# Kernel optimization log

Hardware: AMD Instinct MI355X
Metric: run time of the kernel (lower is better)

The kernel has to match this reference:

```python
import jax, jax.numpy as jnp
import numpy as np

B, N, K = 4, 512, 10
PI_SCALE = 0.05  # keeps sum_k pi in (0, 0.5) so the [1e-8, 1] clamp does not saturate at 1
MCMC_KEY = jax.random.key(42)


def setup_inputs() -> dict:
    key = jax.random.key(0)
    k1, k2, k3, k4 = jax.random.split(key, 4)
    mu = jax.random.normal(k1, (B, N, K), dtype=jnp.float32)
    sig = jax.random.uniform(k2, (B, N, K), dtype=jnp.float32)
    pi = jax.random.uniform(k3, (B, N, K), dtype=jnp.float32) * PI_SCALE
    A_0 = jax.random.uniform(k4, (N, N), dtype=jnp.float32)
    return {"mu": mu, "sig": sig, "pi": pi, "A_0": A_0, "num_samples": 100}


def reference(mu, sig, pi, A_0, num_samples):
    b, n, k = mu.shape

    # Mixture-weighted proposal mean/std:  sum_k softmax(pi)_k * {mu,sig}_k
    component_probs = jax.nn.softmax(pi, axis=-1)          # [B,N,K]
    selected_mu = jnp.sum(component_probs * mu, axis=-1)    # [B,N]
    selected_sig = jnp.sum(component_probs * sig, axis=-1)  # [B,N]

    # edge_probs[b,i,j] = clamp(sum_k pi[b,i,k]) -- constant in j; hoisted out of the loop
    # since it depends only on pi (the torch code recomputes it every step).
    edge_probs = jnp.clip(jnp.sum(pi, axis=2), 1e-8, 1.0)[:, :, None]  # [B,N,1]
    log_ep = jnp.log(edge_probs)                                        # [B,N,1]
    log_1mep = jnp.log(1.0 - edge_probs)                                # [B,N,1]

    def log_likelihood(A):  # A: [B,N,N] -> [N]  (sum over dims 0,1 as in torch)
        return jnp.sum(A * log_ep + (1.0 - A) * log_1mep, axis=(0, 1))

    def step(carry, t):
        current_A, acc = carry
        kk = jax.random.fold_in(MCMC_KEY, t)
        k_noise, k_unif = jax.random.split(kk)
        noise = jax.random.normal(k_noise, (b, n), dtype=selected_mu.dtype)
        proposed_mu = selected_mu + noise * selected_sig              # [B,N]
        # sigmoid of rank-1 outer product: einsum('bnc,bmc->bnm') with c==1
        proposed_A = jax.nn.sigmoid(proposed_mu[:, :, None] * proposed_mu[:, None, :])
        ratio = jnp.mean(jnp.clip(jnp.exp(log_likelihood(proposed_A) - log_likelihood(current_A)), 0.0, 1.0))
        accept = jax.random.uniform(k_unif, (b,)) < ratio             # [B] bool
        current_A = jnp.where(accept[:, None, None], proposed_A, current_A)
        return (current_A, acc + current_A), None

    cur0 = jnp.broadcast_to(A_0, (b, n, n)).astype(mu.dtype)
    acc0 = jnp.zeros((b, n, n), dtype=mu.dtype)
    (_, acc), _ = jax.lax.scan(step, (cur0, acc0), jnp.arange(num_samples))
    return acc / num_samples
```

## Files before the change

### kernel.cpp

```cpp
#include <hip/hip_runtime.h>
#include <stdint.h>

#define T_STEPS 100
#define BB 4
#define NN 512
#define KK 10
#define LOG2E 1.4426950408889634

typedef float f4 __attribute__((ext_vector_type(4)));

__device__ __forceinline__ uint32_t rotl32(uint32_t v, int d) {
  return (v << d) | (v >> (32 - d));
}

__device__ __forceinline__ void tf2x32(uint32_t k0, uint32_t k1,
                                       uint32_t& x0, uint32_t& x1) {
  uint32_t k2 = k0 ^ k1 ^ 0x1BD11BDAu;
  x0 += k0; x1 += k1;
#define TFR(r) { x0 += x1; x1 = rotl32(x1, r); x1 ^= x0; }
  TFR(13) TFR(15) TFR(26) TFR(6)   x0 += k1; x1 += k2 + 1u;
  TFR(17) TFR(29) TFR(16) TFR(24)  x0 += k2; x1 += k0 + 2u;
  TFR(13) TFR(15) TFR(26) TFR(6)   x0 += k0; x1 += k1 + 3u;
  TFR(17) TFR(29) TFR(16) TFR(24)  x0 += k1; x1 += k2 + 4u;
  TFR(13) TFR(15) TFR(26) TFR(6)   x0 += k2; x1 += k0 + 5u;
#undef TFR
}

__device__ __forceinline__ float bits_to_u01(uint32_t bits) {
  return __fsub_rn(__uint_as_float((bits >> 9) | 0x3f800000u), 1.0f);
}

__device__ __forceinline__ float erfinv_f32(float x) {
  float w = -logf(__fmul_rn(__fsub_rn(1.0f, x), __fadd_rn(1.0f, x)));
  float p;
  if (w < 5.0f) {
    w = __fsub_rn(w, 2.5f);
    p = 2.81022636e-08f;
    p = __fadd_rn(__fmul_rn(p, w), 3.43273939e-07f);
    p = __fadd_rn(__fmul_rn(p, w), -3.5233877e-06f);
    p = __fadd_rn(__fmul_rn(p, w), -4.39150654e-06f);
    p = __fadd_rn(__fmul_rn(p, w), 0.00021858087f);
    p = __fadd_rn(__fmul_rn(p, w), -0.00125372503f);
    p = __fadd_rn(__fmul_rn(p, w), -0.00417768164f);
    p = __fadd_rn(__fmul_rn(p, w), 0.246640727f);
    p = __fadd_rn(__fmul_rn(p, w), 1.50140941f);
  } else {
    w = __fsub_rn(sqrtf(w), 3.0f);
    p = -0.000200214257f;
    p = __fadd_rn(__fmul_rn(p, w), 0.000100950558f);
    p = __fadd_rn(__fmul_rn(p, w), 0.00134934322f);
    p = __fadd_rn(__fmul_rn(p, w), -0.00367342844f);
    p = __fadd_rn(__fmul_rn(p, w), 0.00573950773f);
    p = __fadd_rn(__fmul_rn(p, w), -0.0076224613f);
    p = __fadd_rn(__fmul_rn(p, w), 0.00943887047f);
    p = __fadd_rn(__fmul_rn(p, w), 1.00167406f);
    p = __fadd_rn(__fmul_rn(p, w), 2.83297682f);
  }
  return __fmul_rn(p, x);
}

__device__ __forceinline__ float fast_sigmoid(float x) {
  float e = __expf(-x);
  return __builtin_amdgcn_rcpf(__fadd_rn(1.0f, e));
}

template <int CTRL>
__device__ __forceinline__ float dpp_add(float x) {
  int v = __builtin_amdgcn_update_dpp(0, __float_as_int(x), CTRL, 0xF, 0xF, true);
  return __fadd_rn(x, __int_as_float(v));
}
__device__ __forceinline__ float readlane_f(float x, int lane) {
  return __int_as_float(__builtin_amdgcn_readlane(__float_as_int(x), lane));
}

__global__ void rng_kernel(const float* __restrict__ mu,
                           const float* __restrict__ sig,
                           const float* __restrict__ pi,
                           float* __restrict__ pm, float* __restrict__ uacc,
                           float* __restrict__ Lf) {
  int id = blockIdx.x * blockDim.x + threadIdx.x;
  if (id >= T_STEPS * BB * NN) return;
  int t = id >> 11;
  int m = id & 2047;

  const float* pp = pi + m * KK;
  float mx = pp[0];
  for (int k = 1; k < KK; k++) mx = fmaxf(mx, pp[k]);
  float e[KK]; float s = 0.0f;
  for (int k = 0; k < KK; k++) { e[k] = expf(__fsub_rn(pp[k], mx)); s = __fadd_rn(s, e[k]); }
  float smv = 0.0f, ssv = 0.0f, eps = 0.0f;
  for (int k = 0; k < KK; k++) {
    float p = e[k] / s;
    smv = __fadd_rn(smv, __fmul_rn(p, mu[m * KK + k]));
    ssv = __fadd_rn(ssv, __fmul_rn(p, sig[m * KK + k]));
    eps = __fadd_rn(eps, pp[k]);
  }
  if (t == 0) {
    float ep = fminf(fmaxf(eps, 1e-8f), 1.0f);
    float lep = logf(ep);
    float l1 = logf(__fsub_rn(1.0f, ep));
    Lf[m] = (float)((double)lep - (double)l1);
  }

  uint32_t kk0 = 0u, kk1 = (uint32_t)t;
  tf2x32(0u, 42u, kk0, kk1);
  uint32_t n0 = 0u, n1 = 0u; tf2x32(kk0, kk1, n0, n1);
  uint32_t y0 = 0u, y1 = (uint32_t)m;
  tf2x32(n0, n1, y0, y1);
  uint32_t bits = y0 ^ y1;

  float u01 = bits_to_u01(bits);
  const float lo = -0.99999994f;
  float u = fmaxf(lo, __fadd_rn(__fmul_rn(u01, 2.0f), lo));
  float z = __fmul_rn(1.41421356237309515f, erfinv_f32(u));
  pm[id] = __fadd_rn(smv, __fmul_rn(z, ssv));

  if (m < 4) {
    uint32_t u0 = 0u, u1 = 1u; tf2x32(kk0, kk1, u0, u1);
    uint32_t c0 = 0u, c1 = (uint32_t)m;
    tf2x32(u0, u1, c0, c1);
    uacc[t * 4 + m] = __fmul_rn(bits_to_u01(c0 ^ c1), 512.0f);
  }
}

__global__ __launch_bounds__(512) void ll_kernel(const float* __restrict__ pm,
                                                 const float* __restrict__ Lf,
                                                 const float* __restrict__ A0,
                                                 float* __restrict__ llt,
                                                 float* __restrict__ ll0,
                                                 float* __restrict__ tsum) {
  __shared__ float spm[BB][NN];
  __shared__ float sL[BB][NN];
  __shared__ double pt[4][128];
  int tid = threadIdx.x;
  int q = tid >> 7, jj = tid & 127;
  int bi = blockIdx.x;
  if (bi < 400) {
    int t = bi >> 2, jc = bi & 3;
    #pragma unroll
    for (int b = 0; b < BB; b++) {
      spm[b][tid] = pm[(t * 4 + b) * NN + tid];
      sL[b][tid] = Lf[b * NN + tid];
    }
    __syncthreads();
    int i0 = q * 128;
    double tsd = 0.0;
    for (int b = 0; b < BB; b++) {
      float pmj = spm[b][jc * 128 + jj];
      double acc = 0.0;
      #pragma unroll 8
      for (int i = 0; i < 128; i += 2) {
        float x0 = __fmul_rn(spm[b][i0 + i], pmj);
        float x1 = __fmul_rn(spm[b][i0 + i + 1], pmj);
        float t0 = __fmul_rn(fast_sigmoid(x0), sL[b][i0 + i]);
        float t1 = __fmul_rn(fast_sigmoid(x1), sL[b][i0 + i + 1]);
        acc += (double)__fadd_rn(t0, t1);
      }
      pt[q][jj] = acc;
      __syncthreads();
      if (tid < 128) {
        double a = ((pt[0][jj] + pt[1][jj]) + pt[2][jj]) + pt[3][jj];
        llt[(t * 4 + b) * NN + jc * 128 + jj] = (float)(a * LOG2E);
        tsd += a;
      }
      __syncthreads();
    }
    if (tid < 128) tsum[t * NN + jc * 128 + jj] = (float)(tsd * LOG2E);
  } else {
    int idx = bi - 400;
    int b = idx >> 2, jc = idx & 3;
    sL[0][tid] = Lf[b * NN + tid];
    __syncthreads();
    int j = jc * 128 + jj;
    int i0 = q * 128;
    double acc = 0.0;
    #pragma unroll 4
    for (int i = 0; i < 128; i++) {
      acc += (double)A0[(size_t)(i0 + i) * NN + j] * (double)sL[0][i0 + i];
    }
    pt[q][jj] = acc;
    __syncthreads();
    if (tid < 128) {
      double a = ((pt[0][jj] + pt[1][jj]) + pt[2][jj]) + pt[3][jj];
      ll0[b * NN + jc * 128 + jj] = (float)(a * LOG2E);
    }
  }
}

#define CH_LOAD(BUF, T)                                                      \
  {                                                                          \
    BUF##Ts0 = tsv[(size_t)(T) * 128 + g];                                   \
    BUF##Ts1 = tsv[(size_t)(T) * 128 + 64 + g];                              \
    _Pragma("unroll")                                                        \
    for (int b = 0; b < 4; b++) {                                            \
      _Pragma("unroll")                                                      \
      for (int k = 0; k < 2; k++)                                            \
        BUF##R[b * 2 + k] = lltv[((size_t)(T) * 4 + b) * 128 + k * 64 + g];  \
    }                                                                        \
  }

#define CH_STEP(BUF, T)                                                      \
  {                                                                          \
    float4 ua = sua[T];                                                      \
    f4 d0 = BUF##Ts0 - C0;                                                   \
    f4 d1 = BUF##Ts1 - C1;                                                   \
    f4 E0, E1;                                                               \
    _Pragma("unroll")                                                        \
    for (int c = 0; c < 4; c++) {                                            \
      E0[c] = fminf(exp2f(d0[c]), 1.0f);                                     \
      E1[c] = fminf(exp2f(d1[c]), 1.0f);                                     \
    }                                                                        \
    f4 Es = E0 + E1;                                                         \
    float ps = __fadd_rn(__fadd_rn(Es[0], Es[1]), __fadd_rn(Es[2], Es[3]));  \
    ps = dpp_add<0xB1>(ps);                                        \
    ps = dpp_add<0x4E>(ps);                                        \
    ps = dpp_add<0x141>(ps);                         \
    ps = dpp_add<0x140>(ps);                              \
    float s0 = readlane_f(ps, 0), s1 = readlane_f(ps, 16);                   \
    float s2 = readlane_f(ps, 32), s3 = readlane_f(ps, 48);                  \
    float tot = __fadd_rn(__fadd_rn(s0, s1), __fadd_rn(s2, s3));             \
    int am = (ua.x < tot ? 1 : 0) | (ua.y < tot ? 2 : 0) |                   \
             (ua.z < tot ? 4 : 0) | (ua.w < tot ? 8 : 0);                    \
    am = __builtin_amdgcn_readfirstlane(am);                                 \
    if (am) {                                                                \
      if (am & 1) { st0 = (T); cur[0] = BUF##R[0]; cur[1] = BUF##R[1]; }     \
      if (am & 2) { st1 = (T); cur[2] = BUF##R[2]; cur[3] = BUF##R[3]; }     \
      if (am & 4) { st2 = (T); cur[4] = BUF##R[4]; cur[5] = BUF##R[5]; }     \
      if (am & 8) { st3 = (T); cur[6] = BUF##R[6]; cur[7] = BUF##R[7]; }     \
      C0 = (cur[0] + cur[2]) + (cur[4] + cur[6]);                            \
      C1 = (cur[1] + cur[3]) + (cur[5] + cur[7]);                            \
    }                                                                        \
    if (g == 0) {                                                            \
      uint32_t pk = (uint32_t)(st0 + 1) | ((uint32_t)(st1 + 1) << 8) |       \
                    ((uint32_t)(st2 + 1) << 16) | ((uint32_t)(st3 + 1) << 24);\
      spk[T] = pk;                                                           \
    }                                                                        \
  }

__global__ __launch_bounds__(64, 1) void chain_kernel(const float* __restrict__ llt,
                                                      const float* __restrict__ tsum,
                                                      const float* __restrict__ ll0,
                                                      const float* __restrict__ uacc,
                                                      int* __restrict__ slist,
                                                      float* __restrict__ wlist,
                                                      int* __restrict__ Mv) {
  __shared__ float4 sua[T_STEPS];
  __shared__ uint32_t spk[T_STEPS];
  __shared__ int scnt[BB][101];
  int g = threadIdx.x;

  const float4* uacc4 = (const float4*)uacc;
  for (int t = g; t < T_STEPS; t += 64) sua[t] = uacc4[t];

  const f4* lltv = (const f4*)llt;
  const f4* tsv  = (const f4*)tsum;
  const f4* ll0v = (const f4*)ll0;

  f4 cur[8];
  #pragma unroll
  for (int b = 0; b < 4; b++)
    #pragma unroll
    for (int k = 0; k < 2; k++) cur[b * 2 + k] = ll0v[b * 128 + k * 64 + g];
  f4 C0 = (cur[0] + cur[2]) + (cur[4] + cur[6]);
  f4 C1 = (cur[1] + cur[3]) + (cur[5] + cur[7]);
  int st0 = -1, st1 = -1, st2 = -1, st3 = -1;

  f4 ATs0, ATs1, AR[8];
  f4 BTs0, BTs1, BR[8];
  CH_LOAD(A, 0)
  CH_LOAD(B, 1)
  __syncthreads();

  for (int t = 0; t < T_STEPS; t += 2) {
    CH_STEP(A, t)
    if (t + 2 < T_STEPS) CH_LOAD(A, t + 2)
    CH_STEP(B, t + 1)
    if (t + 3 < T_STEPS) CH_LOAD(B, t + 3)
  }

  __syncthreads();
  for (int s = g; s < BB * 101; s += 64) (&scnt[0][0])[s] = 0;
  __syncthreads();
  {
    uint32_t p0 = spk[g];
    atomicAdd(&scnt[0][p0 & 255], 1);
    atomicAdd(&scnt[1][(p0 >> 8) & 255], 1);
    atomicAdd(&scnt[2][(p0 >> 16) & 255], 1);
    atomicAdd(&scnt[3][p0 >> 24], 1);
    if (g < T_STEPS - 64) {
      uint32_t p1 = spk[64 + g];
      atomicAdd(&scnt[0][p1 & 255], 1);
      atomicAdd(&scnt[1][(p1 >> 8) & 255], 1);
      atomicAdd(&scnt[2][(p1 >> 16) & 255], 1);
      atomicAdd(&scnt[3][p1 >> 24], 1);
    }
  }
  __syncthreads();
  if (g < 4) {
    int m = 0;
    for (int s = 0; s <= 100; s++) {
      int c = scnt[g][s];
      if (c) { slist[g * 104 + m] = s; wlist[g * 104 + m] = (float)c; m++; }
    }
    Mv[g] = m;
  }
}

__global__ __launch_bounds__(512) void out_kernel(const float* __restrict__ pm,
                                                  const float* __restrict__ A0,
                                                  const int* __restrict__ slist,
                                                  const float* __restrict__ wlist,
                                                  const int* __restrict__ Mv,
                                                  float* __restrict__ out) {
  int b = blockIdx.x >> 9;
  int i = blockIdx.x & 511;
  int j = threadIdx.x;
  int M = Mv[b];
  float r = 0.0f;
  for (int e = 0; e < M; e++) {
    int s = slist[b * 104 + e];
    float w = wlist[b * 104 + e];
    if (s == 0) {
      r += w * A0[(size_t)i * NN + j];
    } else {
      int t = s - 1;
      float pmi = pm[(size_t)(t * BB + b) * NN + i];
      float pmj = pm[(size_t)(t * BB + b) * NN + j];
      r += w * fast_sigmoid(__fmul_rn(pmi, pmj));
    }
  }
  out[((size_t)b * NN + i) * NN + j] = r * 0.01f;
}

extern "C" void kernel_launch(void* const* d_in, const int* in_sizes, int n_in,
                              void* d_out, int out_size, void* d_ws, size_t ws_size,
                              hipStream_t stream) {
  const float* mu  = (const float*)d_in[0];
  const float* sig = (const float*)d_in[1];
  const float* pi  = (const float*)d_in[2];
  const float* A0  = (const float*)d_in[3];

  char* ws = (char*)d_ws;
  size_t off = 0;
  auto alloc = [&](size_t bytes) -> char* {
    char* p = ws + off;
    off += (bytes + 255) & ~(size_t)255;
    return p;
  };
  float* llt   = (float*)alloc((size_t)T_STEPS * BB * NN * 4);
  float* tsum  = (float*)alloc((size_t)T_STEPS * NN * 4);
  float* ll0   = (float*)alloc(BB * NN * 4);
  float* pm    = (float*)alloc((size_t)T_STEPS * BB * NN * 4);
  float* Lf    = (float*)alloc(BB * NN * 4);
  float* uacc  = (float*)alloc(T_STEPS * 4 * 4);
  int*   slist = (int*)alloc(BB * 104 * 4);
  float* wlist = (float*)alloc(BB * 104 * 4);
  int*   Mv    = (int*)alloc(4 * 4);
  float* outp  = (float*)d_out;

  rng_kernel<<<(T_STEPS * BB * NN + 255) / 256, 256, 0, stream>>>(mu, sig, pi,
                                                                  pm, uacc, Lf);
  ll_kernel<<<416, 512, 0, stream>>>(pm, Lf, A0, llt, ll0, tsum);
  chain_kernel<<<1, 64, 0, stream>>>(llt, tsum, ll0, uacc, slist, wlist, Mv);
  out_kernel<<<BB * NN, 512, 0, stream>>>(pm, A0, slist, wlist, Mv, outp);
}
```

Measured before the change: 155.4 us.

## Fuse RNG into likelihood kernel and process two chain steps speculatively per iteration

Removes the separate rng_kernel by computing the softmax-weighted proposal means, noise, log-odds and uniforms inside ll_kernel's prologue. Each of the four column blocks recomputes this for its timestep, and only jc==0 writes pm. The serial chain kernel now handles steps in pairs. It speculatively evaluates the second step's acceptance ratio for every possible number of batch acceptances in the first step, ordered by uniform rank, so the two wave reductions no longer depend on each other. This cuts a kernel launch and shortens the serial dependency chain, at the cost of redundant RNG/softmax work and about six reductions per pair instead of two.

```diff
diff --git a/kernel.cpp b/kernel.cpp
--- a/kernel.cpp
+++ b/kernel.cpp
@@ -72,60 +72,32 @@
 __device__ __forceinline__ float readlane_f(float x, int lane) {
   return __int_as_float(__builtin_amdgcn_readlane(__float_as_int(x), lane));
 }
-
-__global__ void rng_kernel(const float* __restrict__ mu,
-                           const float* __restrict__ sig,
-                           const float* __restrict__ pi,
-                           float* __restrict__ pm, float* __restrict__ uacc,
-                           float* __restrict__ Lf) {
-  int id = blockIdx.x * blockDim.x + threadIdx.x;
-  if (id >= T_STEPS * BB * NN) return;
-  int t = id >> 11;
-  int m = id & 2047;
-
-  const float* pp = pi + m * KK;
-  float mx = pp[0];
-  for (int k = 1; k < KK; k++) mx = fmaxf(mx, pp[k]);
-  float e[KK]; float s = 0.0f;
-  for (int k = 0; k < KK; k++) { e[k] = expf(__fsub_rn(pp[k], mx)); s = __fadd_rn(s, e[k]); }
-  float smv = 0.0f, ssv = 0.0f, eps = 0.0f;
-  for (int k = 0; k < KK; k++) {
-    float p = e[k] / s;
-    smv = __fadd_rn(smv, __fmul_rn(p, mu[m * KK + k]));
-    ssv = __fadd_rn(ssv, __fmul_rn(p, sig[m * KK + k]));
-    eps = __fadd_rn(eps, pp[k]);
-  }
-  if (t == 0) {
-    float ep = fminf(fmaxf(eps, 1e-8f), 1.0f);
-    float lep = logf(ep);
-    float l1 = logf(__fsub_rn(1.0f, ep));
-    Lf[m] = (float)((double)lep - (double)l1);
-  }
-
-  uint32_t kk0 = 0u, kk1 = (uint32_t)t;
-  tf2x32(0u, 42u, kk0, kk1);
-  uint32_t n0 = 0u, n1 = 0u; tf2x32(kk0, kk1, n0, n1);
-  uint32_t y0 = 0u, y1 = (uint32_t)m;
-  tf2x32(n0, n1, y0, y1);
-  uint32_t bits = y0 ^ y1;
-
-  float u01 = bits_to_u01(bits);
-  const float lo = -0.99999994f;
-  float u = fmaxf(lo, __fadd_rn(__fmul_rn(u01, 2.0f), lo));
-  float z = __fmul_rn(1.41421356237309515f, erfinv_f32(u));
-  pm[id] = __fadd_rn(smv, __fmul_rn(z, ssv));
-
-  if (m < 4) {
-    uint32_t u0 = 0u, u1 = 1u; tf2x32(kk0, kk1, u0, u1);
-    uint32_t c0 = 0u, c1 = (uint32_t)m;
-    tf2x32(u0, u1, c0, c1);
-    uacc[t * 4 + m] = __fmul_rn(bits_to_u01(c0 ^ c1), 512.0f);
-  }
-}
-
-__global__ __launch_bounds__(512) void ll_kernel(const float* __restrict__ pm,
-                                                 const float* __restrict__ Lf,
+__device__ __forceinline__ float wave_tot(float ps) {
+  ps = dpp_add<0xB1>(ps);
+  ps = dpp_add<0x4E>(ps);
+  ps = dpp_add<0x141>(ps);
+  ps = dpp_add<0x140>(ps);
+  float s0 = readlane_f(ps, 0), s1 = readlane_f(ps, 16);
+  float s2 = readlane_f(ps, 32), s3 = readlane_f(ps, 48);
+  return __fadd_rn(__fadd_rn(s0, s1), __fadd_rn(s2, s3));
+}
+__device__ __forceinline__ float eval8(f4 a0, f4 a1) {
+  f4 E0, E1;
+  #pragma unroll
+  for (int c = 0; c < 4; c++) {
+    E0[c] = fminf(exp2f(a0[c]), 1.0f);
+    E1[c] = fminf(exp2f(a1[c]), 1.0f);
+  }
+  f4 Es = E0 + E1;
+  return __fadd_rn(__fadd_rn(Es[0], Es[1]), __fadd_rn(Es[2], Es[3]));
+}
+
+__global__ __launch_bounds__(512) void ll_kernel(const float* __restrict__ mu,
+                                                 const float* __restrict__ sig,
+                                                 const float* __restrict__ pi,
                                                  const float* __restrict__ A0,
+                                                 float* __restrict__ pm,
+                                                 float* __restrict__ uacc,
                                                  float* __restrict__ llt,
                                                  float* __restrict__ ll0,
                                                  float* __restrict__ tsum) {
@@ -137,10 +109,45 @@
   int bi = blockIdx.x;
   if (bi < 400) {
     int t = bi >> 2, jc = bi & 3;
+    uint32_t kk0 = 0u, kk1 = (uint32_t)t;
+    tf2x32(0u, 42u, kk0, kk1);
+    uint32_t n0 = 0u, n1 = 0u; tf2x32(kk0, kk1, n0, n1);
     #pragma unroll
     for (int b = 0; b < BB; b++) {
-      spm[b][tid] = pm[(t * 4 + b) * NN + tid];
-      sL[b][tid] = Lf[b * NN + tid];
+      int m = b * NN + tid;
+      const float* pp = pi + m * KK;
+      float mx = pp[0];
+      for (int k = 1; k < KK; k++) mx = fmaxf(mx, pp[k]);
+      float e[KK]; float s = 0.0f;
+      for (int k = 0; k < KK; k++) { e[k] = expf(__fsub_rn(pp[k], mx)); s = __fadd_rn(s, e[k]); }
+      float smv = 0.0f, ssv = 0.0f, eps = 0.0f;
+      for (int k = 0; k < KK; k++) {
+        float p = e[k] / s;
+        smv = __fadd_rn(smv, __fmul_rn(p, mu[m * KK + k]));
+        ssv = __fadd_rn(ssv, __fmul_rn(p, sig[m * KK + k]));
+        eps = __fadd_rn(eps, pp[k]);
+      }
+      float ep = fminf(fmaxf(eps, 1e-8f), 1.0f);
+      float lep = logf(ep);
+      float l1 = logf(__fsub_rn(1.0f, ep));
+      sL[b][tid] = (float)((double)lep - (double)l1);
+
+      uint32_t y0 = 0u, y1 = (uint32_t)m;
+      tf2x32(n0, n1, y0, y1);
+      uint32_t bits = y0 ^ y1;
+      float u01 = bits_to_u01(bits);
+      const float lo = -0.99999994f;
+      float u = fmaxf(lo, __fadd_rn(__fmul_rn(u01, 2.0f), lo));
+      float z = __fmul_rn(1.41421356237309515f, erfinv_f32(u));
+      float pmv = __fadd_rn(smv, __fmul_rn(z, ssv));
+      spm[b][tid] = pmv;
+      if (jc == 0) pm[(t * 4 + b) * NN + tid] = pmv;
+    }
+    if (jc == 0 && tid < 4) {
+      uint32_t u0 = 0u, u1 = 1u; tf2x32(kk0, kk1, u0, u1);
+      uint32_t c0 = 0u, c1 = (uint32_t)tid;
+      tf2x32(u0, u1, c0, c1);
+      uacc[t * 4 + tid] = __fmul_rn(bits_to_u01(c0 ^ c1), 512.0f);
     }
     __syncthreads();
     int i0 = q * 128;
@@ -169,7 +176,16 @@
   } else {
     int idx = bi - 400;
     int b = idx >> 2, jc = idx & 3;
-    sL[0][tid] = Lf[b * NN + tid];
+    {
+      int m = b * NN + tid;
+      const float* pp = pi + m * KK;
+      float eps = 0.0f;
+      for (int k = 0; k < KK; k++) eps = __fadd_rn(eps, pp[k]);
+      float ep = fminf(fmaxf(eps, 1e-8f), 1.0f);
+      float lep = logf(ep);
+      float l1 = logf(__fsub_rn(1.0f, ep));
+      sL[0][tid] = (float)((double)lep - (double)l1);
+    }
     __syncthreads();
     int j = jc * 128 + jj;
     int i0 = q * 128;
@@ -187,53 +203,99 @@
   }
 }
 
-#define CH_LOAD(BUF, T)                                                      \
+#define PAIR_LOAD(BUF, P)                                                    \
   {                                                                          \
-    BUF##Ts0 = tsv[(size_t)(T) * 128 + g];                                   \
-    BUF##Ts1 = tsv[(size_t)(T) * 128 + 64 + g];                              \
+    int t0_ = 2 * (P), t1_ = t0_ + 1;                                        \
+    BUF##Te0 = tsv[(size_t)t0_ * 128 + g];                                   \
+    BUF##Te1 = tsv[(size_t)t0_ * 128 + 64 + g];                              \
+    BUF##To0 = tsv[(size_t)t1_ * 128 + g];                                   \
+    BUF##To1 = tsv[(size_t)t1_ * 128 + 64 + g];                              \
     _Pragma("unroll")                                                        \
     for (int b = 0; b < 4; b++) {                                            \
       _Pragma("unroll")                                                      \
-      for (int k = 0; k < 2; k++)                                            \
-        BUF##R[b * 2 + k] = lltv[((size_t)(T) * 4 + b) * 128 + k * 64 + g];  \
+      for (int k = 0; k < 2; k++) {                                          \
+        BUF##Re[b * 2 + k] = lltv[((size_t)t0_ * 4 + b) * 128 + k * 64 + g]; \
+        BUF##Ro[b * 2 + k] = lltv[((size_t)t1_ * 4 + b) * 128 + k * 64 + g]; \
+      }                                                                      \
     }                                                                        \
   }
 
-#define CH_STEP(BUF, T)                                                      \
+#define PAIR_STEP(BUF, P)                                                    \
   {                                                                          \
-    float4 ua = sua[T];                                                      \
-    f4 d0 = BUF##Ts0 - C0;                                                   \
-    f4 d1 = BUF##Ts1 - C1;                                                   \
-    f4 E0, E1;                                                               \
-    _Pragma("unroll")                                                        \
-    for (int c = 0; c < 4; c++) {                                            \
-      E0[c] = fminf(exp2f(d0[c]), 1.0f);                                     \
-      E1[c] = fminf(exp2f(d1[c]), 1.0f);                                     \
-    }                                                                        \
-    f4 Es = E0 + E1;                                                         \
-    float ps = __fadd_rn(__fadd_rn(Es[0], Es[1]), __fadd_rn(Es[2], Es[3]));  \
-    ps = dpp_add<0xB1>(ps);                                        \
-    ps = dpp_add<0x4E>(ps);                                        \
-    ps = dpp_add<0x141>(ps);                         \
-    ps = dpp_add<0x140>(ps);                              \
-    float s0 = readlane_f(ps, 0), s1 = readlane_f(ps, 16);                   \
-    float s2 = readlane_f(ps, 32), s3 = readlane_f(ps, 48);                  \
-    float tot = __fadd_rn(__fadd_rn(s0, s1), __fadd_rn(s2, s3));             \
-    int am = (ua.x < tot ? 1 : 0) | (ua.y < tot ? 2 : 0) |                   \
-             (ua.z < tot ? 4 : 0) | (ua.w < tot ? 8 : 0);                    \
-    am = __builtin_amdgcn_readfirstlane(am);                                 \
-    if (am) {                                                                \
-      if (am & 1) { st0 = (T); cur[0] = BUF##R[0]; cur[1] = BUF##R[1]; }     \
-      if (am & 2) { st1 = (T); cur[2] = BUF##R[2]; cur[3] = BUF##R[3]; }     \
-      if (am & 4) { st2 = (T); cur[4] = BUF##R[4]; cur[5] = BUF##R[5]; }     \
-      if (am & 8) { st3 = (T); cur[6] = BUF##R[6]; cur[7] = BUF##R[7]; }     \
+    int t0_ = 2 * (P), t1_ = t0_ + 1;                                        \
+    float4 ue = sua[t0_], uo = sua[t1_];                                     \
+                                          \
+    int re0 = (ue.y < ue.x) + (ue.z < ue.x) + (ue.w < ue.x);                 \
+    int re1 = (ue.x <= ue.y) + (ue.z < ue.y) + (ue.w < ue.y);                \
+    int re2 = (ue.x <= ue.z) + (ue.y <= ue.z) + (ue.w < ue.z);               \
+    int re3 = (ue.x <= ue.w) + (ue.y <= ue.w) + (ue.z <= ue.w);              \
+                                                      \
+    f4 dl0 = BUF##Re[0] - cur[0], dl1 = BUF##Re[1] - cur[1];                 \
+    f4 dl2 = BUF##Re[2] - cur[2], dl3 = BUF##Re[3] - cur[3];                 \
+    f4 dl4 = BUF##Re[4] - cur[4], dl5 = BUF##Re[5] - cur[5];                 \
+    f4 dl6 = BUF##Re[6] - cur[6], dl7 = BUF##Re[7] - cur[7];                 \
+     \
+    f4 z = {};                                                               \
+    f4 p10 = (re0 == 0 ? dl0 : z) + (re1 == 0 ? dl2 : z) +                   \
+             (re2 == 0 ? dl4 : z) + (re3 == 0 ? dl6 : z);                    \
+    f4 p11 = (re0 == 0 ? dl1 : z) + (re1 == 0 ? dl3 : z) +                   \
+             (re2 == 0 ? dl5 : z) + (re3 == 0 ? dl7 : z);                    \
+    f4 p20 = p10 + (re0 == 1 ? dl0 : z) + (re1 == 1 ? dl2 : z) +             \
+             (re2 == 1 ? dl4 : z) + (re3 == 1 ? dl6 : z);                    \
+    f4 p21 = p11 + (re0 == 1 ? dl1 : z) + (re1 == 1 ? dl3 : z) +             \
+             (re2 == 1 ? dl5 : z) + (re3 == 1 ? dl7 : z);                    \
+    f4 p30 = p20 + (re0 == 2 ? dl0 : z) + (re1 == 2 ? dl2 : z) +             \
+             (re2 == 2 ? dl4 : z) + (re3 == 2 ? dl6 : z);                    \
+    f4 p31 = p21 + (re0 == 2 ? dl1 : z) + (re1 == 2 ? dl3 : z) +             \
+             (re2 == 2 ? dl5 : z) + (re3 == 2 ? dl7 : z);                    \
+    f4 p40 = p30 + (re0 == 3 ? dl0 : z) + (re1 == 3 ? dl2 : z) +             \
+             (re2 == 3 ? dl4 : z) + (re3 == 3 ? dl6 : z);                    \
+    f4 p41 = p31 + (re0 == 3 ? dl1 : z) + (re1 == 3 ? dl3 : z) +             \
+             (re2 == 3 ? dl5 : z) + (re3 == 3 ? dl7 : z);                    \
+                                                    \
+    f4 b00 = BUF##Te0 - C0, b01 = BUF##Te1 - C1;                             \
+    f4 b10 = BUF##To0 - C0, b11 = BUF##To1 - C1;                             \
+    float pse  = eval8(b00, b01);                                            \
+    float psc0 = eval8(b10, b11);                                            \
+    float psc1 = eval8(b10 - p10, b11 - p11);                                \
+    float psc2 = eval8(b10 - p20, b11 - p21);                                \
+    float psc3 = eval8(b10 - p30, b11 - p31);                                \
+    float psc4 = eval8(b10 - p40, b11 - p41);                                \
+    float t0v = wave_tot(pse);                                               \
+    float c0v = wave_tot(psc0);                                              \
+    float c1v = wave_tot(psc1);                                              \
+    float c2v = wave_tot(psc2);                                              \
+    float c3v = wave_tot(psc3);                                              \
+    float c4v = wave_tot(psc4);                                              \
+    int kt = (ue.x < t0v) + (ue.y < t0v) + (ue.z < t0v) + (ue.w < t0v);      \
+    kt = __builtin_amdgcn_readfirstlane(kt);                                 \
+    float r1v = kt == 0 ? c0v : kt == 1 ? c1v : kt == 2 ? c2v                \
+              : kt == 3 ? c3v : c4v;                                         \
+    int ko = (uo.x < r1v) + (uo.y < r1v) + (uo.z < r1v) + (uo.w < r1v);      \
+    ko = __builtin_amdgcn_readfirstlane(ko);                                 \
+    int ro0 = (uo.y < uo.x) + (uo.z < uo.x) + (uo.w < uo.x);                 \
+    int ro1 = (uo.x <= uo.y) + (uo.z < uo.y) + (uo.w < uo.y);                \
+    int ro2 = (uo.x <= uo.z) + (uo.y <= uo.z) + (uo.w < uo.z);               \
+    int ro3 = (uo.x <= uo.w) + (uo.y <= uo.w) + (uo.z <= uo.w);              \
+    int sp0 = (re0 < kt) ? t0_ : st0, sp1 = (re1 < kt) ? t0_ : st1;          \
+    int sp2 = (re2 < kt) ? t0_ : st2, sp3 = (re3 < kt) ? t0_ : st3;          \
+    if (kt | ko) {                                                           \
+      if (ro0 < ko)      { st0 = t1_; cur[0] = BUF##Ro[0]; cur[1] = BUF##Ro[1]; } \
+      else if (re0 < kt) { st0 = t0_; cur[0] = BUF##Re[0]; cur[1] = BUF##Re[1]; } \
+      if (ro1 < ko)      { st1 = t1_; cur[2] = BUF##Ro[2]; cur[3] = BUF##Ro[3]; } \
+      else if (re1 < kt) { st1 = t0_; cur[2] = BUF##Re[2]; cur[3] = BUF##Re[3]; } \
+      if (ro2 < ko)      { st2 = t1_; cur[4] = BUF##Ro[4]; cur[5] = BUF##Ro[5]; } \
+      else if (re2 < kt) { st2 = t0_; cur[4] = BUF##Re[4]; cur[5] = BUF##Re[5]; } \
+      if (ro3 < ko)      { st3 = t1_; cur[6] = BUF##Ro[6]; cur[7] = BUF##Ro[7]; } \
+      else if (re3 < kt) { st3 = t0_; cur[6] = BUF##Re[6]; cur[7] = BUF##Re[7]; } \
       C0 = (cur[0] + cur[2]) + (cur[4] + cur[6]);                            \
       C1 = (cur[1] + cur[3]) + (cur[5] + cur[7]);                            \
     }                                                                        \
     if (g == 0) {                                                            \
-      uint32_t pk = (uint32_t)(st0 + 1) | ((uint32_t)(st1 + 1) << 8) |       \
-                    ((uint32_t)(st2 + 1) << 16) | ((uint32_t)(st3 + 1) << 24);\
-      spk[T] = pk;                                                           \
+      spk[t0_] = (uint32_t)(sp0 + 1) | ((uint32_t)(sp1 + 1) << 8) |          \
+                 ((uint32_t)(sp2 + 1) << 16) | ((uint32_t)(sp3 + 1) << 24);  \
+      spk[t1_] = (uint32_t)(st0 + 1) | ((uint32_t)(st1 + 1) << 8) |          \
+                 ((uint32_t)(st2 + 1) << 16) | ((uint32_t)(st3 + 1) << 24);  \
     }                                                                        \
   }
 
@@ -265,17 +327,17 @@
   f4 C1 = (cur[1] + cur[3]) + (cur[5] + cur[7]);
   int st0 = -1, st1 = -1, st2 = -1, st3 = -1;
 
-  f4 ATs0, ATs1, AR[8];
-  f4 BTs0, BTs1, BR[8];
-  CH_LOAD(A, 0)
-  CH_LOAD(B, 1)
+  f4 ATe0, ATe1, ATo0, ATo1, ARe[8], ARo[8];
+  f4 BTe0, BTe1, BTo0, BTo1, BRe[8], BRo[8];
+  PAIR_LOAD(A, 0)
+  PAIR_LOAD(B, 1)
   __syncthreads();
 
-  for (int t = 0; t < T_STEPS; t += 2) {
-    CH_STEP(A, t)
-    if (t + 2 < T_STEPS) CH_LOAD(A, t + 2)
-    CH_STEP(B, t + 1)
-    if (t + 3 < T_STEPS) CH_LOAD(B, t + 3)
+  for (int p = 0; p < 50; p += 2) {
+    PAIR_STEP(A, p)
+    if (p + 2 < 50) PAIR_LOAD(A, p + 2)
+    PAIR_STEP(B, p + 1)
+    if (p + 3 < 50) PAIR_LOAD(B, p + 3)
   }
 
   __syncthreads();
@@ -351,16 +413,13 @@
   float* tsum  = (float*)alloc((size_t)T_STEPS * NN * 4);
   float* ll0   = (float*)alloc(BB * NN * 4);
   float* pm    = (float*)alloc((size_t)T_STEPS * BB * NN * 4);
-  float* Lf    = (float*)alloc(BB * NN * 4);
   float* uacc  = (float*)alloc(T_STEPS * 4 * 4);
   int*   slist = (int*)alloc(BB * 104 * 4);
   float* wlist = (float*)alloc(BB * 104 * 4);
   int*   Mv    = (int*)alloc(4 * 4);
   float* outp  = (float*)d_out;
 
-  rng_kernel<<<(T_STEPS * BB * NN + 255) / 256, 256, 0, stream>>>(mu, sig, pi,
-                                                                  pm, uacc, Lf);
-  ll_kernel<<<416, 512, 0, stream>>>(pm, Lf, A0, llt, ll0, tsum);
+  ll_kernel<<<416, 512, 0, stream>>>(mu, sig, pi, A0, pm, uacc, llt, ll0, tsum);
   chain_kernel<<<1, 64, 0, stream>>>(llt, tsum, ll0, uacc, slist, wlist, Mv);
   out_kernel<<<BB * NN, 512, 0, stream>>>(pm, A0, slist, wlist, Mv, outp);
 }
```

Result: slower. 218.7 us (+40.7%).
